# Kernel optimization log

Hardware: AMD Instinct MI355X
Metric: run time of the kernel (lower is better)

Reference implementation:

```python
import jax, jax.numpy as jnp
import numpy as np

N, E = 50000, 800000
IN_F, HID_F, OUT_F = 128, 128, 32


def setup_inputs() -> dict:
    key = jax.random.key(0)
    ks = jax.random.split(key, 16)
    glorot = lambda k, i, o: jax.random.normal(k, (i, o), jnp.float32) * (2.0 / (i + o)) ** 0.5
    return {
        "x": jax.random.normal(ks[0], (N, IN_F), jnp.float32),
        "src": jax.random.randint(ks[1], (E,), 0, N, jnp.int64),
        "dst": jax.random.randint(ks[2], (E,), 0, N, jnp.int64),
        # layer 0: mean aggregator
        "W_self0": glorot(ks[3], IN_F, HID_F),
        "W_neigh0": glorot(ks[4], IN_F, HID_F),
        "b0": jnp.zeros((HID_F,), jnp.float32),
        # layers 1,2: gcn aggregator (fc_neigh only)
        "W_neigh1": glorot(ks[5], HID_F, HID_F),
        "b1": jnp.zeros((HID_F,), jnp.float32),
        "W_neigh2": glorot(ks[6], HID_F, HID_F),
        "b2": jnp.zeros((HID_F,), jnp.float32),
        # layer 3: mean aggregator
        "W_self3": glorot(ks[7], HID_F, OUT_F),
        "W_neigh3": glorot(ks[8], HID_F, OUT_F),
        "b3": jnp.zeros((OUT_F,), jnp.float32),
    }


def _l2_normalize(x, eps=1e-12):
    # torch F.normalize(x): x / max(||x||_2, eps) along dim 1
    n = jnp.sqrt(jnp.sum(x * x, axis=1, keepdims=True))
    return x / jnp.maximum(n, eps)


def _agg_sum(h, src, dst, n):
    # sum of in-neighbor (src) features onto dst nodes: [N, d]
    return jax.ops.segment_sum(h[src], dst, num_segments=n)


def _sage_mean(h, src, dst, deg, W_self, W_neigh, b):
    nbr = _agg_sum(h, src, dst, h.shape[0]) / jnp.maximum(deg, 1.0)[:, None]
    return h @ W_self + nbr @ W_neigh + b


def _sage_gcn(h, src, dst, deg, W_neigh, b):
    hn = (_agg_sum(h, src, dst, h.shape[0]) + h) / (deg + 1.0)[:, None]
    return hn @ W_neigh + b


def reference(x, src, dst, W_self0, W_neigh0, b0, W_neigh1, b1, W_neigh2, b2,
              W_self3, W_neigh3, b3):
    n = x.shape[0]
    deg = jax.ops.segment_sum(jnp.ones_like(dst, jnp.float32), dst, num_segments=n)
    h = _l2_normalize(x)
    h = jax.nn.relu(_sage_mean(h, src, dst, deg, W_self0, W_neigh0, b0))
    h = jax.nn.relu(_sage_gcn(h, src, dst, deg, W_neigh1, b1))
    h = jax.nn.relu(_sage_gcn(h, src, dst, deg, W_neigh2, b2))
    h = _sage_mean(h, src, dst, deg, W_self3, W_neigh3, b3)  # no relu on last layer
    return h
```

## Files before the change

### kernel.cpp

```cpp
#include <hip/hip_runtime.h>

#define NN 50000
#define NE 800000
#define F  128
#define FO 32

#define RSH  8
#define RSZ  256
#define NBKT 196
#define CAP  5120
#define CAP16 9216
#define PCHUNK 4096
#define NPB  ((NE + PCHUNK - 1) / PCHUNK)
#define MG   ((NN + 63) / 64)
#define LGRID ((NN + 3) / 4)

typedef _Float16 h16;
typedef h16   half8 __attribute__((ext_vector_type(8)));
typedef h16   h16x4 __attribute__((ext_vector_type(4)));
typedef h16   h16x2 __attribute__((ext_vector_type(2)));
typedef float f32x4 __attribute__((ext_vector_type(4)));

__device__ __forceinline__ void wprep_one(const float* __restrict__ W,
        h16* __restrict__ Wf, int idx, int NC, int NCT) {
    if (idx >= 128 * NC) return;
    int k = idx / NC, n = idx - k * NC;
    int kt = k >> 5, g = (k & 31) >> 3, j = k & 7;
    int ct = n >> 4;
    int lane = g * 16 + (n & 15);
    float w = W[idx];
    h16 hi = (h16)w;
    h16 lo = (h16)(w - (float)hi);
    int base = ((kt * NCT + ct) * 64 + lane) * 8 + j;
    Wf[base] = hi;
    Wf[base + NCT * 2048] = lo;
}

__global__ __launch_bounds__(256) void k_pre0(
        const float* __restrict__ S0, const float* __restrict__ N0,
        const float* __restrict__ N1, const float* __restrict__ N2,
        const float* __restrict__ S3, const float* __restrict__ N3,
        h16* fS0, h16* fN0, h16* fN1, h16* fN2, h16* fS3, h16* fN3,
        int* __restrict__ bcur, h16* __restrict__ ghA, h16* __restrict__ ghB,
        h16* __restrict__ gh4) {
    int bb = blockIdx.x, tid = threadIdx.x;
    if (bb < 256) {
        const float* W = bb < 64 ? S0 : bb < 128 ? N0 : bb < 192 ? N1 : N2;
        h16*        Wf = bb < 64 ? fS0 : bb < 128 ? fN0 : bb < 192 ? fN1 : fN2;
        wprep_one(W, Wf, (bb & 63) * 256 + tid, 128, 8);
    } else if (bb < 288) {
        int b2 = bb - 256;
        const float* W = b2 < 16 ? S3 : N3;
        h16*        Wf = b2 < 16 ? fS3 : fN3;
        wprep_one(W, Wf, (b2 & 15) * 256 + tid, 32, 2);
    } else {
        if (tid < NBKT) bcur[tid] = 0;
        if (tid < F) {
            ghA[(size_t)NN * F + tid] = (h16)0.f;
            ghB[(size_t)NN * F + tid] = (h16)0.f;
        }
        if (tid < FO) gh4[(size_t)NN * FO + tid] = (h16)0.f;
    }
}

__global__ __launch_bounds__(256) void k_pre1(const int* __restrict__ src,
        const int* __restrict__ dst, int* __restrict__ bcur, int* __restrict__ barea,
        const float* __restrict__ x, h16* __restrict__ hhi, h16* __restrict__ hlo) {
    __shared__ int cnt[NBKT];
    __shared__ int base[NBKT];
    const int tid = threadIdx.x;
    if ((int)blockIdx.x < NPB) {
        const int e0 = blockIdx.x * PCHUNK;
        for (int i = tid; i < NBKT; i += 256) cnt[i] = 0;
        __syncthreads();
        #pragma unroll
        for (int k = 0; k < PCHUNK / 256; ++k) {
            int e = e0 + k * 256 + tid;
            if (e < NE) atomicAdd(&cnt[dst[e] >> RSH], 1);
        }
        __syncthreads();
        for (int i = tid; i < NBKT; i += 256)
            base[i] = atomicAdd(&bcur[i], cnt[i]);
        __syncthreads();
        for (int i = tid; i < NBKT; i += 256) cnt[i] = base[i];
        __syncthreads();
        #pragma unroll
        for (int k = 0; k < PCHUNK / 256; ++k) {
            int e = e0 + k * 256 + tid;
            if (e < NE) {
                int d = dst[e], sv = src[e];
                int b = d >> RSH;
                int p = atomicAdd(&cnt[b], 1);
                barea[b * CAP + p] = ((d & (RSZ - 1)) << 16) | sv;
            }
        }
    } else {
        const int bb   = blockIdx.x - NPB;
        const int wid  = bb * 4 + (tid >> 6);
        const int lane = tid & 63;
        if (wid >= NN) return;
        const float2* xr = (const float2*)(x + (size_t)wid * F);
        float2 v = xr[lane];
        float ss = v.x * v.x + v.y * v.y;
        #pragma unroll
        for (int d = 1; d < 64; d <<= 1) ss += __shfl_xor(ss, d, 64);
        float inv = 1.0f / fmaxf(sqrtf(ss), 1e-12f);
        float ox = v.x * inv, oy = v.y * inv;
        h16 hx = (h16)ox, hy = (h16)oy;
        h16x2 vhi = {hx, hy};
        h16x2 vlo = {(h16)(ox - (float)hx), (h16)(oy - (float)hy)};
        *(h16x2*)(hhi + (size_t)wid * F + lane * 2) = vhi;
        *(h16x2*)(hlo + (size_t)wid * F + lane * 2) = vlo;
    }
}

template<int NCT, bool OUT16>
__device__ __forceinline__ void mfma_cols(const half8* Ahi, const half8* Alo,
        const h16* __restrict__ Wf, void* __restrict__ out, int row0, int l) {
    const int cdc = l & 15;
    const int cdr = (l >> 4) * 4;
    #pragma unroll
    for (int ct = 0; ct < NCT; ++ct) {
        f32x4 acc = {0.f, 0.f, 0.f, 0.f};
        #pragma unroll
        for (int kt = 0; kt < 4; ++kt) {
            half8 bh = *(const half8*)(Wf + (size_t)(((kt * NCT + ct) * 64 + l) * 8));
            half8 bl = *(const half8*)(Wf + (size_t)((((4 + kt) * NCT + ct) * 64 + l) * 8));
            acc = __builtin_amdgcn_mfma_f32_16x16x32_f16(Ahi[kt], bh, acc, 0, 0, 0);
            acc = __builtin_amdgcn_mfma_f32_16x16x32_f16(Alo[kt], bh, acc, 0, 0, 0);
            acc = __builtin_amdgcn_mfma_f32_16x16x32_f16(Ahi[kt], bl, acc, 0, 0, 0);
        }
        #pragma unroll
        for (int r = 0; r < 4; ++r) {
            int gr = row0 + cdr + r;
            if (gr < NN) {
                size_t oi = (size_t)gr * (NCT * 16) + ct * 16 + cdc;
                if constexpr (OUT16) ((h16*)out)[oi] = (h16)acc[r];
                else                 ((float*)out)[oi] = acc[r];
            }
        }
    }
}

template<int NCTA, int NCTB>
__device__ __forceinline__ void mfma_block(int blk, int tid,
        const h16* __restrict__ hhi, const h16* __restrict__ hlo,
        const h16* __restrict__ WfA, const h16* __restrict__ WfB,
        h16* __restrict__ outA, h16* __restrict__ outB) {
    const int l  = tid & 63;
    const int wv = tid >> 6;
    const int row0 = blk * 64 + wv * 16;
    int ar = row0 + (l & 15); if (ar >= NN) ar = NN - 1;
    const size_t ab = (size_t)ar * F + (l >> 4) * 8;
    half8 Ahi[4], Alo[4];
    #pragma unroll
    for (int kt = 0; kt < 4; ++kt) {
        Ahi[kt] = *(const half8*)(hhi + ab + kt * 32);
        Alo[kt] = *(const half8*)(hlo + ab + kt * 32);
    }
    mfma_cols<NCTA, true>(Ahi, Alo, WfA, (void*)outA, row0, l);
    if constexpr (NCTB > 0) mfma_cols<NCTB, true>(Ahi, Alo, WfB, (void*)outB, row0, l);
}

template<int NCTA, int NCTB>
__global__ __launch_bounds__(256) void k_mfma(const h16* __restrict__ hhi,
        const h16* __restrict__ hlo, const h16* __restrict__ WfA,
        const h16* __restrict__ WfB, h16* __restrict__ outA,
        h16* __restrict__ outB) {
    mfma_block<NCTA, NCTB>(blockIdx.x, threadIdx.x, hhi, hlo, WfA, WfB, outA, outB);
}

__global__ __launch_bounds__(256) void k_bfill_mfma(
        const int* __restrict__ barea, const int* __restrict__ bcur,
        int* __restrict__ offs, float* __restrict__ degf, int* __restrict__ csr,
        const h16* __restrict__ hhi, const h16* __restrict__ hlo,
        const h16* __restrict__ WfA, const h16* __restrict__ WfB,
        h16* __restrict__ outA, h16* __restrict__ outB) {
    __shared__ int hist[RSZ];
    __shared__ int ws[4];
    const int tid = threadIdx.x;
    if ((int)blockIdx.x < NBKT) {
        const int r = blockIdx.x;
        const int lane = tid & 63, wv = tid >> 6;
        const int nb = bcur[r];
        hist[tid] = 0;
        __syncthreads();
        const int* area = barea + r * CAP;
        for (int i = tid; i < nb; i += 256) atomicAdd(&hist[area[i] >> 16], 1);
        __syncthreads();
        const int v   = hist[tid];
        const int psz = (v + 15) & ~15;
        int incl = psz;
        #pragma unroll
        for (int d = 1; d < 64; d <<= 1) {
            int t = __shfl_up(incl, d, 64);
            if (lane >= d) incl += t;
        }
        if (lane == 63) ws[wv] = incl;
        __syncthreads();
        if (tid == 0) {
            int run = 0;
            #pragma unroll
            for (int w = 0; w < 4; ++w) { int t = ws[w]; ws[w] = run; run += t; }
        }
        __syncthreads();
        const int beg  = r * CAP16 + ws[wv] + incl - psz;
        const int node = (r << RSH) + tid;
        if (node < NN) {
            offs[node] = beg;
            degf[node] = (float)v;
        }
        __syncthreads();
        hist[tid] = beg;
        __syncthreads();
        for (int i = tid; i < nb; i += 256) {
            int pk = area[i];
            int p = atomicAdd(&hist[pk >> 16], 1);
            csr[p] = pk & 0xFFFF;
        }
        for (int i = v; i < psz; ++i) csr[beg + i] = NN;
    } else {
        mfma_block<8, 8>((int)blockIdx.x - NBKT, tid, hhi, hlo, WfA, WfB, outA, outB);
    }
}

template<int MODE>
__global__ __launch_bounds__(256) void k_agg128(const h16* __restrict__ g,
        const h16* __restrict__ s, const int* __restrict__ offs,
        const int* __restrict__ csr, const float* __restrict__ degf,
        const float* __restrict__ b, h16* __restrict__ hhi, h16* __restrict__ hlo) {
    const int wid  = (int)((blockIdx.x * 256 + threadIdx.x) >> 6);
    const int lane = threadIdx.x & 63;
    if (wid >= NN) return;
    const int q  = lane >> 4;
    const int li = lane & 15;
    const int beg = offs[wid];
    const float dgf = degf[wid];
    const int n16 = ((int)dgf + 15) >> 4;
    const half8* g8 = (const half8*)g;
    float a0[8], a1[8];
    #pragma unroll
    for (int j = 0; j < 8; ++j) { a0[j] = 0.f; a1[j] = 0.f; }
    for (int t = 0; t < n16; ++t) {
        const int e = beg + (t << 4);
        int u0 = csr[e + q];
        int u1 = csr[e + 4 + q];
        int u2 = csr[e + 8 + q];
        int u3 = csr[e + 12 + q];
        half8 v0 = g8[(size_t)u0 * 16 + li];
        half8 v1 = g8[(size_t)u1 * 16 + li];
        half8 v2 = g8[(size_t)u2 * 16 + li];
        half8 v3 = g8[(size_t)u3 * 16 + li];
        #pragma unroll
        for (int j = 0; j < 8; ++j) {
            a0[j] += (float)v0[j] + (float)v2[j];
            a1[j] += (float)v1[j] + (float)v3[j];
        }
    }
    #pragma unroll
    for (int j = 0; j < 8; ++j) {
        a0[j] += a1[j];
        a0[j] += __shfl_xor(a0[j], 16, 64);
        a0[j] += __shfl_xor(a0[j], 32, 64);
    }
    if (q) return;
    float bb[8];
    *(float4*)(bb)     = *(const float4*)(b + li * 8);
    *(float4*)(bb + 4) = *(const float4*)(b + li * 8 + 4);
    float r[8];
    if (MODE == 0) {
        float inv = 1.f / fmaxf(dgf, 1.f);
        half8 sv = ((const half8*)s)[(size_t)wid * 16 + li];
        #pragma unroll
        for (int j = 0; j < 8; ++j)
            r[j] = fmaxf((float)sv[j] + a0[j] * inv + bb[j], 0.f);
    } else {
        float inv = 1.f / (dgf + 1.f);
        half8 gv = g8[(size_t)wid * 16 + li];
        #pragma unroll
        for (int j = 0; j < 8; ++j)
            r[j] = fmaxf((a0[j] + (float)gv[j]) * inv + bb[j], 0.f);
    }
    half8 vhi, vlo;
    #pragma unroll
    for (int j = 0; j < 8; ++j) {
        h16 hi = (h16)r[j];
        vhi[j] = hi;
        vlo[j] = (h16)(r[j] - (float)hi);
    }
    *(half8*)(hhi + (size_t)wid * F + li * 8) = vhi;
    *(half8*)(hlo + (size_t)wid * F + li * 8) = vlo;
}

__global__ __launch_bounds__(256) void k_agg32(const h16* __restrict__ g,
        const h16* __restrict__ s, const int* __restrict__ offs,
        const int* __restrict__ csr, const float* __restrict__ degf,
        const float* __restrict__ b, float* __restrict__ out) {
    const int wid  = (int)((blockIdx.x * 256 + threadIdx.x) >> 6);
    const int lane = threadIdx.x & 63;
    if (wid >= NN) return;
    const int grp = lane >> 3;
    const int li  = lane & 7;
    const int beg = offs[wid];
    const float dgf = degf[wid];
    const int n16 = ((int)dgf + 15) >> 4;
    const h16x4* g4 = (const h16x4*)g;
    float a0[4] = {0.f, 0.f, 0.f, 0.f}, a1[4] = {0.f, 0.f, 0.f, 0.f};
    for (int t = 0; t < n16; ++t) {
        const int e = beg + (t << 4);
        int u0 = csr[e + grp], u1 = csr[e + 8 + grp];
        h16x4 v0 = g4[(size_t)u0 * 8 + li];
        h16x4 v1 = g4[(size_t)u1 * 8 + li];
        #pragma unroll
        for (int j = 0; j < 4; ++j) { a0[j] += (float)v0[j]; a1[j] += (float)v1[j]; }
    }
    #pragma unroll
    for (int j = 0; j < 4; ++j) {
        a0[j] += a1[j];
        a0[j] += __shfl_xor(a0[j], 8, 64);
        a0[j] += __shfl_xor(a0[j], 16, 64);
        a0[j] += __shfl_xor(a0[j], 32, 64);
    }
    if (grp) return;
    const float inv = 1.f / fmaxf(dgf, 1.f);
    float4 bb = ((const float4*)b)[li];
    h16x4 sv = ((const h16x4*)s)[(size_t)wid * 8 + li];
    float4 r;
    r.x = (float)sv[0] + a0[0] * inv + bb.x;
    r.y = (float)sv[1] + a0[1] * inv + bb.y;
    r.z = (float)sv[2] + a0[2] * inv + bb.z;
    r.w = (float)sv[3] + a0[3] * inv + bb.w;
    ((float4*)out)[(size_t)wid * 8 + li] = r;
}

extern "C" void kernel_launch(void* const* d_in, const int* in_sizes, int n_in,
                              void* d_out, int out_size, void* d_ws, size_t ws_size,
                              hipStream_t stream) {
    const float* x       = (const float*)d_in[0];
    const int*   src     = (const int*)  d_in[1];
    const int*   dst     = (const int*)  d_in[2];
    const float* Wself0  = (const float*)d_in[3];
    const float* Wneigh0 = (const float*)d_in[4];
    const float* b0      = (const float*)d_in[5];
    const float* Wneigh1 = (const float*)d_in[6];
    const float* b1      = (const float*)d_in[7];
    const float* Wneigh2 = (const float*)d_in[8];
    const float* b2      = (const float*)d_in[9];
    const float* Wself3  = (const float*)d_in[10];
    const float* Wneigh3 = (const float*)d_in[11];
    const float* b3      = (const float*)d_in[12];
    float* out = (float*)d_out;

    char* ws = (char*)d_ws;
    size_t off = 0;
    auto alloc = [&](size_t bytes) -> void* {
        void* p = ws + off;
        off += (bytes + 255) & ~(size_t)255;
        return p;
    };
    float* degf   = (float*)alloc((size_t)NN * 4);
    int*   offs   = (int*)  alloc((size_t)(NN + 1) * 4);
    int*   csr    = (int*)  alloc((size_t)NBKT * CAP16 * 4);
    int*   bcur   = (int*)  alloc((size_t)NBKT * 4);
    int*   barea  = (int*)  alloc((size_t)NBKT * CAP * 4);
    h16*   hhi    = (h16*)  alloc((size_t)NN * F * 2);
    h16*   hlo    = (h16*)  alloc((size_t)NN * F * 2);
    h16*   s16    = (h16*)  alloc((size_t)NN * F * 2);
    h16*   ghA    = (h16*)  alloc((size_t)(NN + 1) * F * 2);
    h16*   ghB    = (h16*)  alloc((size_t)(NN + 1) * F * 2);
    h16*   s16b   = (h16*)  alloc((size_t)NN * FO * 2);
    h16*   gh4    = (h16*)  alloc((size_t)(NN + 1) * FO * 2);
    h16*   WfS0   = (h16*)  alloc((size_t)128 * 128 * 2 * 2);
    h16*   WfN0   = (h16*)  alloc((size_t)128 * 128 * 2 * 2);
    h16*   WfN1   = (h16*)  alloc((size_t)128 * 128 * 2 * 2);
    h16*   WfN2   = (h16*)  alloc((size_t)128 * 128 * 2 * 2);
    h16*   WfS3   = (h16*)  alloc((size_t)128 * 32 * 2 * 2);
    h16*   WfN3   = (h16*)  alloc((size_t)128 * 32 * 2 * 2);

    k_pre0<<<289, 256, 0, stream>>>(Wself0, Wneigh0, Wneigh1, Wneigh2,
                                    Wself3, Wneigh3,
                                    WfS0, WfN0, WfN1, WfN2, WfS3, WfN3,
                                    bcur, ghA, ghB, gh4);
    k_pre1<<<NPB + LGRID, 256, 0, stream>>>(src, dst, bcur, barea, x, hhi, hlo);
    k_bfill_mfma<<<NBKT + MG, 256, 0, stream>>>(barea, bcur, offs, degf, csr,
                                                hhi, hlo, WfS0, WfN0, s16, ghA);
    k_agg128<0><<<LGRID, 256, 0, stream>>>(ghA, s16, offs, csr, degf, b0, hhi, hlo);
    k_mfma<8, 0><<<MG, 256, 0, stream>>>(hhi, hlo, WfN1, nullptr, ghB, nullptr);
    k_agg128<1><<<LGRID, 256, 0, stream>>>(ghB, nullptr, offs, csr, degf, b1, hhi, hlo);
    k_mfma<8, 0><<<MG, 256, 0, stream>>>(hhi, hlo, WfN2, nullptr, ghA, nullptr);
    k_agg128<1><<<LGRID, 256, 0, stream>>>(ghA, nullptr, offs, csr, degf, b2, hhi, hlo);
    k_mfma<2, 2><<<MG, 256, 0, stream>>>(hhi, hlo, WfS3, WfN3, s16b, gh4);
    k_agg32<<<LGRID, 256, 0, stream>>>(gh4, s16b, offs, csr, degf, b3, out);
}
```

Before: 297.0 us.

## Split 128-wide aggregation into four feature quarters across separate blocks

The 128-feature gather-aggregate kernel is launched with four times as many blocks. Each block handles one 32-feature quarter of a node, so each wave processes 16 edges per step with 4 lanes per edge row instead of 4 edges with 16 lanes. The aim is more parallelism and fewer serial iterations per node, at the cost of reading each CSR index and degree four times and doing two extra shuffle stages. Each gathered row now splits into 64-byte segments, which may hurt gather efficiency and cache locality across the quarter blocks.

```diff
diff --git a/kernel.cpp b/kernel.cpp
--- a/kernel.cpp
+++ b/kernel.cpp
@@ -225,71 +225,74 @@
 }
 
 template<int MODE>
-__global__ __launch_bounds__(256) void k_agg128(const h16* __restrict__ g,
+__global__ __launch_bounds__(256) void k_agg128q(const h16* __restrict__ g,
         const h16* __restrict__ s, const int* __restrict__ offs,
         const int* __restrict__ csr, const float* __restrict__ degf,
         const float* __restrict__ b, h16* __restrict__ hhi, h16* __restrict__ hlo) {
-    const int wid  = (int)((blockIdx.x * 256 + threadIdx.x) >> 6);
+    const int bq  = blockIdx.x / LGRID;
+    const int bb  = blockIdx.x - bq * LGRID;
+    const int wid = bb * 4 + (threadIdx.x >> 6);
     const int lane = threadIdx.x & 63;
     if (wid >= NN) return;
-    const int q  = lane >> 4;
-    const int li = lane & 15;
+    const int r = lane >> 2;
+    const int c = lane & 3;
     const int beg = offs[wid];
     const float dgf = degf[wid];
     const int n16 = ((int)dgf + 15) >> 4;
-    const half8* g8 = (const half8*)g;
+    const half8* gq = (const half8*)g + bq * 4 + c;
     float a0[8], a1[8];
     #pragma unroll
     for (int j = 0; j < 8; ++j) { a0[j] = 0.f; a1[j] = 0.f; }
-    for (int t = 0; t < n16; ++t) {
-        const int e = beg + (t << 4);
-        int u0 = csr[e + q];
-        int u1 = csr[e + 4 + q];
-        int u2 = csr[e + 8 + q];
-        int u3 = csr[e + 12 + q];
-        half8 v0 = g8[(size_t)u0 * 16 + li];
-        half8 v1 = g8[(size_t)u1 * 16 + li];
-        half8 v2 = g8[(size_t)u2 * 16 + li];
-        half8 v3 = g8[(size_t)u3 * 16 + li];
-        #pragma unroll
-        for (int j = 0; j < 8; ++j) {
-            a0[j] += (float)v0[j] + (float)v2[j];
-            a1[j] += (float)v1[j] + (float)v3[j];
-        }
+    int t = 0;
+    for (; t + 2 <= n16; t += 2) {
+        int u0 = csr[beg + t * 16 + r];
+        int u1 = csr[beg + t * 16 + 16 + r];
+        half8 v0 = gq[(size_t)u0 * 16];
+        half8 v1 = gq[(size_t)u1 * 16];
+        #pragma unroll
+        for (int j = 0; j < 8; ++j) { a0[j] += (float)v0[j]; a1[j] += (float)v1[j]; }
+    }
+    if (t < n16) {
+        int u0 = csr[beg + t * 16 + r];
+        half8 v0 = gq[(size_t)u0 * 16];
+        #pragma unroll
+        for (int j = 0; j < 8; ++j) a0[j] += (float)v0[j];
     }
     #pragma unroll
     for (int j = 0; j < 8; ++j) {
         a0[j] += a1[j];
+        a0[j] += __shfl_xor(a0[j], 4, 64);
+        a0[j] += __shfl_xor(a0[j], 8, 64);
         a0[j] += __shfl_xor(a0[j], 16, 64);
         a0[j] += __shfl_xor(a0[j], 32, 64);
     }
-    if (q) return;
-    float bb[8];
-    *(float4*)(bb)     = *(const float4*)(b + li * 8);
-    *(float4*)(bb + 4) = *(const float4*)(b + li * 8 + 4);
-    float r[8];
+    if (r) return;
+    float bb8[8];
+    *(float4*)(bb8)     = *(const float4*)(b + bq * 32 + c * 8);
+    *(float4*)(bb8 + 4) = *(const float4*)(b + bq * 32 + c * 8 + 4);
+    float rr[8];
     if (MODE == 0) {
         float inv = 1.f / fmaxf(dgf, 1.f);
-        half8 sv = ((const half8*)s)[(size_t)wid * 16 + li];
+        half8 sv = ((const half8*)s)[(size_t)wid * 16 + bq * 4 + c];
         #pragma unroll
         for (int j = 0; j < 8; ++j)
-            r[j] = fmaxf((float)sv[j] + a0[j] * inv + bb[j], 0.f);
+            rr[j] = fmaxf((float)sv[j] + a0[j] * inv + bb8[j], 0.f);
     } else {
         float inv = 1.f / (dgf + 1.f);
-        half8 gv = g8[(size_t)wid * 16 + li];
+        half8 gv = gq[(size_t)wid * 16];
         #pragma unroll
         for (int j = 0; j < 8; ++j)
-            r[j] = fmaxf((a0[j] + (float)gv[j]) * inv + bb[j], 0.f);
+            rr[j] = fmaxf((a0[j] + (float)gv[j]) * inv + bb8[j], 0.f);
     }
     half8 vhi, vlo;
     #pragma unroll
     for (int j = 0; j < 8; ++j) {
-        h16 hi = (h16)r[j];
+        h16 hi = (h16)rr[j];
         vhi[j] = hi;
-        vlo[j] = (h16)(r[j] - (float)hi);
-    }
-    *(half8*)(hhi + (size_t)wid * F + li * 8) = vhi;
-    *(half8*)(hlo + (size_t)wid * F + li * 8) = vlo;
+        vlo[j] = (h16)(rr[j] - (float)hi);
+    }
+    *(half8*)(hhi + (size_t)wid * F + bq * 32 + c * 8) = vhi;
+    *(half8*)(hlo + (size_t)wid * F + bq * 32 + c * 8) = vlo;
 }
 
 __global__ __launch_bounds__(256) void k_agg32(const h16* __restrict__ g,
@@ -384,11 +387,11 @@
     k_pre1<<<NPB + LGRID, 256, 0, stream>>>(src, dst, bcur, barea, x, hhi, hlo);
     k_bfill_mfma<<<NBKT + MG, 256, 0, stream>>>(barea, bcur, offs, degf, csr,
                                                 hhi, hlo, WfS0, WfN0, s16, ghA);
-    k_agg128<0><<<LGRID, 256, 0, stream>>>(ghA, s16, offs, csr, degf, b0, hhi, hlo);
+    k_agg128q<0><<<4 * LGRID, 256, 0, stream>>>(ghA, s16, offs, csr, degf, b0, hhi, hlo);
     k_mfma<8, 0><<<MG, 256, 0, stream>>>(hhi, hlo, WfN1, nullptr, ghB, nullptr);
-    k_agg128<1><<<LGRID, 256, 0, stream>>>(ghB, nullptr, offs, csr, degf, b1, hhi, hlo);
+    k_agg128q<1><<<4 * LGRID, 256, 0, stream>>>(ghB, nullptr, offs, csr, degf, b1, hhi, hlo);
     k_mfma<8, 0><<<MG, 256, 0, stream>>>(hhi, hlo, WfN2, nullptr, ghA, nullptr);
-    k_agg128<1><<<LGRID, 256, 0, stream>>>(ghA, nullptr, offs, csr, degf, b2, hhi, hlo);
+    k_agg128q<1><<<4 * LGRID, 256, 0, stream>>>(ghA, nullptr, offs, csr, degf, b2, hhi, hlo);
     k_mfma<2, 2><<<MG, 256, 0, stream>>>(hhi, hlo, WfS3, WfN3, s16b, gh4);
     k_agg32<<<LGRID, 256, 0, stream>>>(gh4, s16b, offs, csr, degf, b3, out);
 }
```

Measured after the change: 409.6 us. 37.9% more time.

## Fuse neighbor aggregation with following MFMA GEMM and normalize into layer-0 GEMM

Applied to the files above, without the earlier changes.

The L2-normalize step now feeds the layer-0 self and neighbor GEMMs directly inside k_pre1, so they are no longer a separate pass through an intermediate hi/lo buffer. The 128-wide aggregation kernels are merged with the next layer's MFMA GEMM, which removes the hhi/hlo round trips and three kernel launches. In the fused kernel each lane gathers full neighbor lists for one node row in the 16-row MFMA A layout. This duplicates CSR index loads across the four k-slices and serializes each row's gather within a lane, so latency hiding and load balance may suffer compared with the previous wave-per-node gather.

```diff
diff --git a/kernel.cpp b/kernel.cpp
--- a/kernel.cpp
+++ b/kernel.cpp
@@ -18,7 +18,6 @@
 typedef _Float16 h16;
 typedef h16   half8 __attribute__((ext_vector_type(8)));
 typedef h16   h16x4 __attribute__((ext_vector_type(4)));
-typedef h16   h16x2 __attribute__((ext_vector_type(2)));
 typedef float f32x4 __attribute__((ext_vector_type(4)));
 
 __device__ __forceinline__ void wprep_one(const float* __restrict__ W,
@@ -63,9 +62,38 @@
     }
 }
 
+template<int NCT, bool OUT16>
+__device__ __forceinline__ void mfma_cols(const half8* Ahi, const half8* Alo,
+        const h16* __restrict__ Wf, void* __restrict__ out, int row0, int l) {
+    const int cdc = l & 15;
+    const int cdr = (l >> 4) * 4;
+    #pragma unroll
+    for (int ct = 0; ct < NCT; ++ct) {
+        f32x4 acc = {0.f, 0.f, 0.f, 0.f};
+        #pragma unroll
+        for (int kt = 0; kt < 4; ++kt) {
+            half8 bh = *(const half8*)(Wf + (size_t)(((kt * NCT + ct) * 64 + l) * 8));
+            half8 bl = *(const half8*)(Wf + (size_t)((((4 + kt) * NCT + ct) * 64 + l) * 8));
+            acc = __builtin_amdgcn_mfma_f32_16x16x32_f16(Ahi[kt], bh, acc, 0, 0, 0);
+            acc = __builtin_amdgcn_mfma_f32_16x16x32_f16(Alo[kt], bh, acc, 0, 0, 0);
+            acc = __builtin_amdgcn_mfma_f32_16x16x32_f16(Ahi[kt], bl, acc, 0, 0, 0);
+        }
+        #pragma unroll
+        for (int r = 0; r < 4; ++r) {
+            int gr = row0 + cdr + r;
+            if (gr < NN) {
+                size_t oi = (size_t)gr * (NCT * 16) + ct * 16 + cdc;
+                if constexpr (OUT16) ((h16*)out)[oi] = (h16)acc[r];
+                else                 ((float*)out)[oi] = acc[r];
+            }
+        }
+    }
+}
+
 __global__ __launch_bounds__(256) void k_pre1(const int* __restrict__ src,
         const int* __restrict__ dst, int* __restrict__ bcur, int* __restrict__ barea,
-        const float* __restrict__ x, h16* __restrict__ hhi, h16* __restrict__ hlo) {
+        const float* __restrict__ x, const h16* __restrict__ WfS0,
+        const h16* __restrict__ WfN0, h16* __restrict__ s16, h16* __restrict__ gh) {
     __shared__ int cnt[NBKT];
     __shared__ int base[NBKT];
     const int tid = threadIdx.x;
@@ -95,201 +123,145 @@
             }
         }
     } else {
-        const int bb   = blockIdx.x - NPB;
-        const int wid  = bb * 4 + (tid >> 6);
-        const int lane = tid & 63;
-        if (wid >= NN) return;
-        const float2* xr = (const float2*)(x + (size_t)wid * F);
-        float2 v = xr[lane];
-        float ss = v.x * v.x + v.y * v.y;
-        #pragma unroll
-        for (int d = 1; d < 64; d <<= 1) ss += __shfl_xor(ss, d, 64);
+        const int bb = (int)blockIdx.x - NPB;
+        const int l  = tid & 63, wv = tid >> 6;
+        const int row0 = bb * 64 + wv * 16;
+        int nd = row0 + (l & 15); if (nd >= NN) nd = NN - 1;
+        const int ks = l >> 4;
+        float v[4][8];
+        #pragma unroll
+        for (int kt = 0; kt < 4; ++kt) {
+            const float* xr = x + (size_t)nd * F + kt * 32 + ks * 8;
+            *(float4*)(&v[kt][0]) = *(const float4*)(xr);
+            *(float4*)(&v[kt][4]) = *(const float4*)(xr + 4);
+        }
+        float ss = 0.f;
+        #pragma unroll
+        for (int kt = 0; kt < 4; ++kt)
+            #pragma unroll
+            for (int j = 0; j < 8; ++j) ss += v[kt][j] * v[kt][j];
+        ss += __shfl_xor(ss, 16, 64);
+        ss += __shfl_xor(ss, 32, 64);
         float inv = 1.0f / fmaxf(sqrtf(ss), 1e-12f);
-        float ox = v.x * inv, oy = v.y * inv;
-        h16 hx = (h16)ox, hy = (h16)oy;
-        h16x2 vhi = {hx, hy};
-        h16x2 vlo = {(h16)(ox - (float)hx), (h16)(oy - (float)hy)};
-        *(h16x2*)(hhi + (size_t)wid * F + lane * 2) = vhi;
-        *(h16x2*)(hlo + (size_t)wid * F + lane * 2) = vlo;
-    }
-}
-
-template<int NCT, bool OUT16>
-__device__ __forceinline__ void mfma_cols(const half8* Ahi, const half8* Alo,
-        const h16* __restrict__ Wf, void* __restrict__ out, int row0, int l) {
-    const int cdc = l & 15;
-    const int cdr = (l >> 4) * 4;
-    #pragma unroll
-    for (int ct = 0; ct < NCT; ++ct) {
-        f32x4 acc = {0.f, 0.f, 0.f, 0.f};
-        #pragma unroll
-        for (int kt = 0; kt < 4; ++kt) {
-            half8 bh = *(const half8*)(Wf + (size_t)(((kt * NCT + ct) * 64 + l) * 8));
-            half8 bl = *(const half8*)(Wf + (size_t)((((4 + kt) * NCT + ct) * 64 + l) * 8));
-            acc = __builtin_amdgcn_mfma_f32_16x16x32_f16(Ahi[kt], bh, acc, 0, 0, 0);
-            acc = __builtin_amdgcn_mfma_f32_16x16x32_f16(Alo[kt], bh, acc, 0, 0, 0);
-            acc = __builtin_amdgcn_mfma_f32_16x16x32_f16(Ahi[kt], bl, acc, 0, 0, 0);
-        }
-        #pragma unroll
-        for (int r = 0; r < 4; ++r) {
-            int gr = row0 + cdr + r;
-            if (gr < NN) {
-                size_t oi = (size_t)gr * (NCT * 16) + ct * 16 + cdc;
-                if constexpr (OUT16) ((h16*)out)[oi] = (h16)acc[r];
-                else                 ((float*)out)[oi] = acc[r];
+        half8 Ahi[4], Alo[4];
+        #pragma unroll
+        for (int kt = 0; kt < 4; ++kt)
+            #pragma unroll
+            for (int j = 0; j < 8; ++j) {
+                float o = v[kt][j] * inv;
+                h16 hi = (h16)o;
+                Ahi[kt][j] = hi;
+                Alo[kt][j] = (h16)(o - (float)hi);
             }
-        }
-    }
-}
-
-template<int NCTA, int NCTB>
-__device__ __forceinline__ void mfma_block(int blk, int tid,
-        const h16* __restrict__ hhi, const h16* __restrict__ hlo,
+        mfma_cols<8, true>(Ahi, Alo, WfS0, (void*)s16, row0, l);
+        mfma_cols<8, true>(Ahi, Alo, WfN0, (void*)gh, row0, l);
+    }
+}
+
+__global__ __launch_bounds__(256) void k_bfill(const int* __restrict__ barea,
+        const int* __restrict__ bcur, int* __restrict__ offs,
+        float* __restrict__ degf, int* __restrict__ csr) {
+    __shared__ int hist[RSZ];
+    __shared__ int ws[4];
+    const int r = blockIdx.x, tid = threadIdx.x;
+    const int lane = tid & 63, wv = tid >> 6;
+    const int nb = bcur[r];
+    hist[tid] = 0;
+    __syncthreads();
+    const int* area = barea + r * CAP;
+    for (int i = tid; i < nb; i += 256) atomicAdd(&hist[area[i] >> 16], 1);
+    __syncthreads();
+    const int v   = hist[tid];
+    const int psz = (v + 15) & ~15;
+    int incl = psz;
+    #pragma unroll
+    for (int d = 1; d < 64; d <<= 1) {
+        int t = __shfl_up(incl, d, 64);
+        if (lane >= d) incl += t;
+    }
+    if (lane == 63) ws[wv] = incl;
+    __syncthreads();
+    if (tid == 0) {
+        int run = 0;
+        #pragma unroll
+        for (int w = 0; w < 4; ++w) { int t = ws[w]; ws[w] = run; run += t; }
+    }
+    __syncthreads();
+    const int beg  = r * CAP16 + ws[wv] + incl - psz;
+    const int node = (r << RSH) + tid;
+    if (node < NN) {
+        offs[node] = beg;
+        degf[node] = (float)v;
+    }
+    __syncthreads();
+    hist[tid] = beg;
+    __syncthreads();
+    for (int i = tid; i < nb; i += 256) {
+        int pk = area[i];
+        int p = atomicAdd(&hist[pk >> 16], 1);
+        csr[p] = pk & 0xFFFF;
+    }
+    for (int i = v; i < psz; ++i) csr[beg + i] = NN;
+}
+
+template<int MODE, int NCTA, int NCTB>
+__global__ __launch_bounds__(256) void k_fusedA(const h16* __restrict__ g,
+        const h16* __restrict__ s, const int* __restrict__ offs,
+        const int* __restrict__ csr, const float* __restrict__ degf,
+        const float* __restrict__ bias,
         const h16* __restrict__ WfA, const h16* __restrict__ WfB,
         h16* __restrict__ outA, h16* __restrict__ outB) {
-    const int l  = tid & 63;
-    const int wv = tid >> 6;
-    const int row0 = blk * 64 + wv * 16;
-    int ar = row0 + (l & 15); if (ar >= NN) ar = NN - 1;
-    const size_t ab = (size_t)ar * F + (l >> 4) * 8;
+    const int tid = threadIdx.x;
+    const int l = tid & 63, wv = tid >> 6;
+    const int row0 = blockIdx.x * 64 + wv * 16;
+    int nd = row0 + (l & 15); if (nd >= NN) nd = NN - 1;
+    const int ks = l >> 4;
+    const int beg = offs[nd];
+    const float dgf = degf[nd];
+    const int dpad = ((int)dgf + 15) & ~15;
+    const half8* g8 = (const half8*)g;
+    const int2* csr2 = (const int2*)(csr + beg);
+    float a[4][8];
+    #pragma unroll
+    for (int kt = 0; kt < 4; ++kt)
+        #pragma unroll
+        for (int j = 0; j < 8; ++j) a[kt][j] = 0.f;
+    for (int e = 0; e < dpad; e += 2) {
+        int2 uu = csr2[e >> 1];
+        size_t b0 = (size_t)uu.x * 16 + ks;
+        size_t b1 = (size_t)uu.y * 16 + ks;
+        half8 p00 = g8[b0], p01 = g8[b0 + 4], p02 = g8[b0 + 8], p03 = g8[b0 + 12];
+        half8 p10 = g8[b1], p11 = g8[b1 + 4], p12 = g8[b1 + 8], p13 = g8[b1 + 12];
+        #pragma unroll
+        for (int j = 0; j < 8; ++j) {
+            a[0][j] += (float)p00[j] + (float)p10[j];
+            a[1][j] += (float)p01[j] + (float)p11[j];
+            a[2][j] += (float)p02[j] + (float)p12[j];
+            a[3][j] += (float)p03[j] + (float)p13[j];
+        }
+    }
+    const float inv = (MODE == 0) ? 1.f / fmaxf(dgf, 1.f) : 1.f / (dgf + 1.f);
     half8 Ahi[4], Alo[4];
     #pragma unroll
     for (int kt = 0; kt < 4; ++kt) {
-        Ahi[kt] = *(const half8*)(hhi + ab + kt * 32);
-        Alo[kt] = *(const half8*)(hlo + ab + kt * 32);
+        float bb[8];
+        *(float4*)(bb)     = *(const float4*)(bias + kt * 32 + ks * 8);
+        *(float4*)(bb + 4) = *(const float4*)(bias + kt * 32 + ks * 8 + 4);
+        half8 sv;
+        if constexpr (MODE == 0) sv = ((const half8*)s)[(size_t)nd * 16 + kt * 4 + ks];
+        else                     sv = g8[(size_t)nd * 16 + kt * 4 + ks];
+        #pragma unroll
+        for (int j = 0; j < 8; ++j) {
+            float r;
+            if constexpr (MODE == 0) r = fmaxf((float)sv[j] + a[kt][j] * inv + bb[j], 0.f);
+            else                     r = fmaxf((a[kt][j] + (float)sv[j]) * inv + bb[j], 0.f);
+            h16 hi = (h16)r;
+            Ahi[kt][j] = hi;
+            Alo[kt][j] = (h16)(r - (float)hi);
+        }
     }
     mfma_cols<NCTA, true>(Ahi, Alo, WfA, (void*)outA, row0, l);
     if constexpr (NCTB > 0) mfma_cols<NCTB, true>(Ahi, Alo, WfB, (void*)outB, row0, l);
-}
-
-template<int NCTA, int NCTB>
-__global__ __launch_bounds__(256) void k_mfma(const h16* __restrict__ hhi,
-        const h16* __restrict__ hlo, const h16* __restrict__ WfA,
-        const h16* __restrict__ WfB, h16* __restrict__ outA,
-        h16* __restrict__ outB) {
-    mfma_block<NCTA, NCTB>(blockIdx.x, threadIdx.x, hhi, hlo, WfA, WfB, outA, outB);
-}
-
-__global__ __launch_bounds__(256) void k_bfill_mfma(
-        const int* __restrict__ barea, const int* __restrict__ bcur,
-        int* __restrict__ offs, float* __restrict__ degf, int* __restrict__ csr,
-        const h16* __restrict__ hhi, const h16* __restrict__ hlo,
-        const h16* __restrict__ WfA, const h16* __restrict__ WfB,
-        h16* __restrict__ outA, h16* __restrict__ outB) {
-    __shared__ int hist[RSZ];
-    __shared__ int ws[4];
-    const int tid = threadIdx.x;
-    if ((int)blockIdx.x < NBKT) {
-        const int r = blockIdx.x;
-        const int lane = tid & 63, wv = tid >> 6;
-        const int nb = bcur[r];
-        hist[tid] = 0;
-        __syncthreads();
-        const int* area = barea + r * CAP;
-        for (int i = tid; i < nb; i += 256) atomicAdd(&hist[area[i] >> 16], 1);
-        __syncthreads();
-        const int v   = hist[tid];
-        const int psz = (v + 15) & ~15;
-        int incl = psz;
-        #pragma unroll
-        for (int d = 1; d < 64; d <<= 1) {
-            int t = __shfl_up(incl, d, 64);
-            if (lane >= d) incl += t;
-        }
-        if (lane == 63) ws[wv] = incl;
-        __syncthreads();
-        if (tid == 0) {
-            int run = 0;
-            #pragma unroll
-            for (int w = 0; w < 4; ++w) { int t = ws[w]; ws[w] = run; run += t; }
-        }
-        __syncthreads();
-        const int beg  = r * CAP16 + ws[wv] + incl - psz;
-        const int node = (r << RSH) + tid;
-        if (node < NN) {
-            offs[node] = beg;
-            degf[node] = (float)v;
-        }
-        __syncthreads();
-        hist[tid] = beg;
-        __syncthreads();
-        for (int i = tid; i < nb; i += 256) {
-            int pk = area[i];
-            int p = atomicAdd(&hist[pk >> 16], 1);
-            csr[p] = pk & 0xFFFF;
-        }
-        for (int i = v; i < psz; ++i) csr[beg + i] = NN;
-    } else {
-        mfma_block<8, 8>((int)blockIdx.x - NBKT, tid, hhi, hlo, WfA, WfB, outA, outB);
-    }
-}
-
-template<int MODE>
-__global__ __launch_bounds__(256) void k_agg128(const h16* __restrict__ g,
-        const h16* __restrict__ s, const int* __restrict__ offs,
-        const int* __restrict__ csr, const float* __restrict__ degf,
-        const float* __restrict__ b, h16* __restrict__ hhi, h16* __restrict__ hlo) {
-    const int wid  = (int)((blockIdx.x * 256 + threadIdx.x) >> 6);
-    const int lane = threadIdx.x & 63;
-    if (wid >= NN) return;
-    const int q  = lane >> 4;
-    const int li = lane & 15;
-    const int beg = offs[wid];
-    const float dgf = degf[wid];
-    const int n16 = ((int)dgf + 15) >> 4;
-    const half8* g8 = (const half8*)g;
-    float a0[8], a1[8];
-    #pragma unroll
-    for (int j = 0; j < 8; ++j) { a0[j] = 0.f; a1[j] = 0.f; }
-    for (int t = 0; t < n16; ++t) {
-        const int e = beg + (t << 4);
-        int u0 = csr[e + q];
-        int u1 = csr[e + 4 + q];
-        int u2 = csr[e + 8 + q];
-        int u3 = csr[e + 12 + q];
-        half8 v0 = g8[(size_t)u0 * 16 + li];
-        half8 v1 = g8[(size_t)u1 * 16 + li];
-        half8 v2 = g8[(size_t)u2 * 16 + li];
-        half8 v3 = g8[(size_t)u3 * 16 + li];
-        #pragma unroll
-        for (int j = 0; j < 8; ++j) {
-            a0[j] += (float)v0[j] + (float)v2[j];
-            a1[j] += (float)v1[j] + (float)v3[j];
-        }
-    }
-    #pragma unroll
-    for (int j = 0; j < 8; ++j) {
-        a0[j] += a1[j];
-        a0[j] += __shfl_xor(a0[j], 16, 64);
-        a0[j] += __shfl_xor(a0[j], 32, 64);
-    }
-    if (q) return;
-    float bb[8];
-    *(float4*)(bb)     = *(const float4*)(b + li * 8);
-    *(float4*)(bb + 4) = *(const float4*)(b + li * 8 + 4);
-    float r[8];
-    if (MODE == 0) {
-        float inv = 1.f / fmaxf(dgf, 1.f);
-        half8 sv = ((const half8*)s)[(size_t)wid * 16 + li];
-        #pragma unroll
-        for (int j = 0; j < 8; ++j)
-            r[j] = fmaxf((float)sv[j] + a0[j] * inv + bb[j], 0.f);
-    } else {
-        float inv = 1.f / (dgf + 1.f);
-        half8 gv = g8[(size_t)wid * 16 + li];
-        #pragma unroll
-        for (int j = 0; j < 8; ++j)
-            r[j] = fmaxf((a0[j] + (float)gv[j]) * inv + bb[j], 0.f);
-    }
-    half8 vhi, vlo;
-    #pragma unroll
-    for (int j = 0; j < 8; ++j) {
-        h16 hi = (h16)r[j];
-        vhi[j] = hi;
-        vlo[j] = (h16)(r[j] - (float)hi);
-    }
-    *(half8*)(hhi + (size_t)wid * F + li * 8) = vhi;
-    *(half8*)(hlo + (size_t)wid * F + li * 8) = vlo;
 }
 
 __global__ __launch_bounds__(256) void k_agg32(const h16* __restrict__ g,
@@ -363,8 +335,6 @@
     int*   csr    = (int*)  alloc((size_t)NBKT * CAP16 * 4);
     int*   bcur   = (int*)  alloc((size_t)NBKT * 4);
     int*   barea  = (int*)  alloc((size_t)NBKT * CAP * 4);
-    h16*   hhi    = (h16*)  alloc((size_t)NN * F * 2);
-    h16*   hlo    = (h16*)  alloc((size_t)NN * F * 2);
     h16*   s16    = (h16*)  alloc((size_t)NN * F * 2);
     h16*   ghA    = (h16*)  alloc((size_t)(NN + 1) * F * 2);
     h16*   ghB    = (h16*)  alloc((size_t)(NN + 1) * F * 2);
@@ -381,14 +351,14 @@
                                     Wself3, Wneigh3,
                                     WfS0, WfN0, WfN1, WfN2, WfS3, WfN3,
                                     bcur, ghA, ghB, gh4);
-    k_pre1<<<NPB + LGRID, 256, 0, stream>>>(src, dst, bcur, barea, x, hhi, hlo);
-    k_bfill_mfma<<<NBKT + MG, 256, 0, stream>>>(barea, bcur, offs, degf, csr,
-                                                hhi, hlo, WfS0, WfN0, s16, ghA);
-    k_agg128<0><<<LGRID, 256, 0, stream>>>(ghA, s16, offs, csr, degf, b0, hhi, hlo);
-    k_mfma<8, 0><<<MG, 256, 0, stream>>>(hhi, hlo, WfN1, nullptr, ghB, nullptr);
-    k_agg128<1><<<LGRID, 256, 0, stream>>>(ghB, nullptr, offs, csr, degf, b1, hhi, hlo);
-    k_mfma<8, 0><<<MG, 256, 0, stream>>>(hhi, hlo, WfN2, nullptr, ghA, nullptr);
-    k_agg128<1><<<LGRID, 256, 0, stream>>>(ghA, nullptr, offs, csr, degf, b2, hhi, hlo);
-    k_mfma<2, 2><<<MG, 256, 0, stream>>>(hhi, hlo, WfS3, WfN3, s16b, gh4);
+    k_pre1<<<NPB + MG, 256, 0, stream>>>(src, dst, bcur, barea, x,
+                                         WfS0, WfN0, s16, ghA);
+    k_bfill<<<NBKT, 256, 0, stream>>>(barea, bcur, offs, degf, csr);
+    k_fusedA<0, 8, 0><<<MG, 256, 0, stream>>>(ghA, s16, offs, csr, degf, b0,
+                                              WfN1, nullptr, ghB, nullptr);
+    k_fusedA<1, 8, 0><<<MG, 256, 0, stream>>>(ghB, nullptr, offs, csr, degf, b1,
+                                              WfN2, nullptr, ghA, nullptr);
+    k_fusedA<1, 2, 2><<<MG, 256, 0, stream>>>(ghA, nullptr, offs, csr, degf, b2,
+                                              WfS3, WfN3, s16b, gh4);
     k_agg32<<<LGRID, 256, 0, stream>>>(gh4, s16b, offs, csr, degf, b3, out);
 }
```

Measured after the change: 317.6 us. +6.9%, slower.
